# Optimization experiments

Measured on AMD Instinct MI355X. Metric: run time of the kernel, lower is better.

The kernel has to match this reference:

```python
import jax, jax.numpy as jnp
import numpy as np

M, N, DIM = 256, 256, 512
NUM_EPOCHS = 100
ALPHA = 0.3
SIGMA = max(M, N) / 2.0


def _neuron_locations(m, n):
    ii, jj = jnp.meshgrid(jnp.arange(m), jnp.arange(n), indexing='ij')
    return jnp.stack([ii.reshape(-1), jj.reshape(-1)], axis=1)  # [m*n, 2] int32


def setup_inputs() -> dict:
    key = jax.random.key(0)
    k1, k2 = jax.random.split(key)
    input_vector = jax.random.normal(k1, (DIM,), dtype=jnp.float32)
    weights = jax.random.normal(k2, (M * N, DIM), dtype=jnp.float32)
    epoch = 10
    return {"input_vector": input_vector, "weights": weights, "epoch": epoch}


def reference(input_vector, weights, epoch):
    locs = _neuron_locations(M, N)  # [m*n, 2]
    # --- BMU search: broadcast distance + argmin (no tiling needed) ---
    diff = weights - input_vector[None, :]                  # [m*n, dim]
    distance = jnp.sqrt(jnp.sum(diff * diff, axis=1))       # [m*n]
    bmu_index = jnp.argmin(distance)
    bmu_loc = locs[bmu_index]                               # [2]
    # --- training update ---
    epoch_f = jnp.float32(epoch)
    learning_rate = 1.0 - epoch_f / NUM_EPOCHS
    alpha_op = ALPHA * learning_rate
    sigma_op = SIGMA * learning_rate
    loc_diff = locs - bmu_loc[None, :]                      # [m*n, 2]
    bmu_dist_sq = jnp.sum(loc_diff * loc_diff, axis=1).astype(jnp.float32)  # [m*n]
    neighbourhood = jnp.exp(-bmu_dist_sq / (sigma_op * sigma_op))
    lr_mult = (alpha_op * neighbourhood)[:, None]           # [m*n, 1]
    new_weights = weights + lr_mult * (input_vector[None, :] - weights)
    return bmu_loc, new_weights
```

## Files before the change

kernel.cpp:

```cpp
#include <hip/hip_runtime.h>

#define SOM_M 256
#define SOM_N 256
#define SOM_DIM 512
#define SOM_ROWS (SOM_M * SOM_N)
#define SOM_ELEMS (SOM_ROWS * SOM_DIM)
#define NB 2048

typedef float f32x4 __attribute__((ext_vector_type(4)));
typedef float f32x2 __attribute__((ext_vector_type(2)));

__global__ __launch_bounds__(256) void som_bmu_partial(
    const float* __restrict__ w, const float* __restrict__ in,
    unsigned long long* __restrict__ part) {
  __shared__ float s_in[SOM_DIM];
  for (int i = threadIdx.x; i < SOM_DIM; i += 256) s_in[i] = in[i];
  __syncthreads();

  const int wave = threadIdx.x >> 6;
  const int lane = threadIdx.x & 63;
  const int globalWave = blockIdx.x * 4 + wave;
  const int nWaves = NB * 4;

  float bd = 3.4e38f;
  int bi = SOM_ROWS;

  const f32x4* in4 = (const f32x4*)s_in;
  for (int row = globalWave; row < SOM_ROWS; row += nWaves) {
    const f32x4* wr = (const f32x4*)(w + (size_t)row * SOM_DIM);
    float acc = 0.f;
#pragma unroll
    for (int k = 0; k < 2; ++k) {
      f32x4 wv = wr[lane + 64 * k];
      f32x4 iv = in4[lane + 64 * k];
      f32x4 d = wv - iv;
      acc += d.x * d.x + d.y * d.y + d.z * d.z + d.w * d.w;
    }
#pragma unroll
    for (int off = 32; off; off >>= 1) acc += __shfl_xor(acc, off, 64);
    if (acc < bd) { bd = acc; bi = row; }
  }

  unsigned long long pk =
      ((unsigned long long)__float_as_uint(bd) << 32) | (unsigned int)bi;

  __shared__ unsigned long long sp[4];
  if (lane == 0) sp[wave] = pk;
  __syncthreads();
  if (threadIdx.x == 0) {
    unsigned long long m = sp[0];
#pragma unroll
    for (int k = 1; k < 4; ++k) m = (sp[k] < m) ? sp[k] : m;
    part[blockIdx.x] = m;
  }
}

__global__ __launch_bounds__(256) void som_update(
    const float* __restrict__ w, const float* __restrict__ in,
    const int* __restrict__ epoch_p,
    const unsigned long long* __restrict__ part,
    float* __restrict__ out ) {
  __shared__ unsigned long long sp[256];
  unsigned long long m = ~0ull;
  for (int i = threadIdx.x; i < NB; i += 256) {
    unsigned long long v = part[i];
    m = (v < m) ? v : m;
  }
  sp[threadIdx.x] = m;
  __syncthreads();
  for (int s = 128; s; s >>= 1) {
    if ((int)threadIdx.x < s) {
      if (sp[threadIdx.x + s] < sp[threadIdx.x]) sp[threadIdx.x] = sp[threadIdx.x + s];
    }
    __syncthreads();
  }
  const int bidx = (int)(unsigned int)(sp[0] & 0xFFFFFFFFull);
  const int br = bidx >> 8;
  const int bc = bidx & 255;

  if (blockIdx.x == 0 && threadIdx.x == 0) {
    out[0] = (float)br;
    out[1] = (float)bc;
  }

  const float lr = 1.0f - (float)epoch_p[0] / 100.0f;
  const float alpha_op = 0.3f * lr;
  const float sigma_op = 128.0f * lr;
  const float inv_s2 = 1.0f / (sigma_op * sigma_op);

  const f32x2* w2 = (const f32x2*)w;
  const f32x2* in2 = (const f32x2*)in;
  f32x2* o2 = (f32x2*)(out + 2);

  const int total2 = SOM_ELEMS / 2;
  const int stride = NB * 256;
  for (int j = blockIdx.x * 256 + threadIdx.x; j < total2; j += stride) {
    const int row = j >> 8;
    const int rr = (row >> 8) - br;
    const int cc = (row & 255) - bc;
    const float d2 = (float)(rr * rr + cc * cc);
    const float mult = alpha_op * __expf(-d2 * inv_s2);

    f32x2 wv = w2[j];
    f32x2 iv = in2[j & 255];
    f32x2 r = wv + mult * (iv - wv);
    o2[j] = r;
  }
}

extern "C" void kernel_launch(void* const* d_in, const int* in_sizes, int n_in,
                              void* d_out, int out_size, void* d_ws, size_t ws_size,
                              hipStream_t stream) {
  const float* input_vector = (const float*)d_in[0];
  const float* weights = (const float*)d_in[1];
  const int* epoch = (const int*)d_in[2];
  float* out = (float*)d_out;

  unsigned long long* part = (unsigned long long*)d_ws;

  som_bmu_partial<<<NB, 256, 0, stream>>>(weights, input_vector, part);
  som_update<<<NB, 256, 0, stream>>>(weights, input_vector, epoch, part, out);
}
```

Baseline: 69.08 us.

## Fuse BMU search and update into one cooperative kernel holding weights on-chip

Replaces the two-kernel pipeline with a single cooperative-launch kernel. Each wave loads its 32 weight rows once, computes their distances, and keeps the rows in registers (23 rows) and LDS (9 rows). A grid-wide sync and a reduction of the per-wave partial minima then produce the winning neuron, and the update is written from the on-chip copy. This avoids reading the 128MB weight matrix a second time, at the cost of heavy register and LDS pressure, a grid barrier, and reliance on all 512 blocks being co-resident; the old two-kernel path remains as a fallback if the cooperative launch fails.

```diff
diff --git a/kernel.cpp b/kernel.cpp
--- a/kernel.cpp
+++ b/kernel.cpp
@@ -1,30 +1,135 @@
 #include <hip/hip_runtime.h>
-
-#define SOM_M 256
-#define SOM_N 256
+#include <hip/hip_cooperative_groups.h>
+
+namespace cg = cooperative_groups;
+
 #define SOM_DIM 512
-#define SOM_ROWS (SOM_M * SOM_N)
+#define SOM_ROWS 65536
 #define SOM_ELEMS (SOM_ROWS * SOM_DIM)
-#define NB 2048
+
+#define FGRID 512
+#define FWAVES 4
+#define FROWS_PER_WAVE 32
+#define FLDS_ROWS 9
+#define FREG_ROWS 23
+#define FDYN_LDS (FWAVES * FLDS_ROWS * SOM_DIM * 4)
 
 typedef float f32x4 __attribute__((ext_vector_type(4)));
 typedef float f32x2 __attribute__((ext_vector_type(2)));
 
+__global__ __launch_bounds__(256, 2) void som_fused(
+    const float* __restrict__ w, const float* __restrict__ in,
+    const int* __restrict__ epoch_p,
+    unsigned long long* __restrict__ part,
+    float* __restrict__ out) {
+  extern __shared__ float lds[];
+  const int wave = threadIdx.x >> 6;
+  const int lane = threadIdx.x & 63;
+  const int row0 = blockIdx.x * (FWAVES * FROWS_PER_WAVE) + wave * FROWS_PER_WAVE;
+
+  const f32x4* in4 = (const f32x4*)in;
+  const f32x4 iv0 = in4[lane];
+  const f32x4 iv1 = in4[lane + 64];
+
+  float* wlds = lds + wave * (FLDS_ROWS * SOM_DIM);
+
+  float bd = 3.4e38f;
+  int bi = SOM_ROWS;
+  f32x4 d0[FREG_ROWS], d1[FREG_ROWS];
+
+#pragma unroll
+  for (int r = 0; r < FROWS_PER_WAVE; ++r) {
+    const f32x4* wr = (const f32x4*)(w + (size_t)(row0 + r) * SOM_DIM);
+    f32x4 wv0 = wr[lane];
+    f32x4 wv1 = wr[lane + 64];
+    f32x4 e0 = wv0 - iv0;
+    f32x4 e1 = wv1 - iv1;
+    float acc = e0.x * e0.x + e0.y * e0.y + e0.z * e0.z + e0.w * e0.w +
+                e1.x * e1.x + e1.y * e1.y + e1.z * e1.z + e1.w * e1.w;
+#pragma unroll
+    for (int off = 32; off; off >>= 1) acc += __shfl_xor(acc, off, 64);
+    if (acc < bd) { bd = acc; bi = row0 + r; }
+    if (r < FLDS_ROWS) {
+      f32x4* dst = (f32x4*)(wlds + r * SOM_DIM);
+      dst[lane] = wv0;
+      dst[lane + 64] = wv1;
+    } else {
+      d0[r - FLDS_ROWS] = wv0;
+      d1[r - FLDS_ROWS] = wv1;
+    }
+  }
+
+  if (lane == 0) {
+    part[blockIdx.x * FWAVES + wave] =
+        ((unsigned long long)__float_as_uint(bd) << 32) | (unsigned int)bi;
+  }
+
+  cg::this_grid().sync();
+
+  unsigned long long m = part[lane];
+#pragma unroll
+  for (int k = 1; k < 32; ++k) {
+    unsigned long long v = part[lane + 64 * k];
+    m = (v < m) ? v : m;
+  }
+#pragma unroll
+  for (int off = 32; off; off >>= 1) {
+    unsigned long long v = __shfl_xor(m, off, 64);
+    m = (v < m) ? v : m;
+  }
+  const int bidx = (int)(unsigned int)(m & 0xFFFFFFFFull);
+  const int br = bidx >> 8;
+  const int bc = bidx & 255;
+
+  if (blockIdx.x == 0 && threadIdx.x == 0) {
+    out[0] = (float)br;
+    out[1] = (float)bc;
+  }
+
+  const float lr = 1.0f - (float)epoch_p[0] * 0.01f;
+  const float alpha_op = 0.3f * lr;
+  const float sigma_op = 128.0f * lr;
+  const float inv_s2 = 1.0f / (sigma_op * sigma_op);
+
+#pragma unroll
+  for (int r = 0; r < FROWS_PER_WAVE; ++r) {
+    const int row = row0 + r;
+    const int rr = (row >> 8) - br;
+    const int cc = (row & 255) - bc;
+    const float mult = alpha_op * __expf(-(float)(rr * rr + cc * cc) * inv_s2);
+    f32x4 wv0, wv1;
+    if (r < FLDS_ROWS) {
+      const f32x4* src = (const f32x4*)(wlds + r * SOM_DIM);
+      wv0 = src[lane];
+      wv1 = src[lane + 64];
+    } else {
+      wv0 = d0[r - FLDS_ROWS];
+      wv1 = d1[r - FLDS_ROWS];
+    }
+    f32x4 r0 = wv0 + mult * (iv0 - wv0);
+    f32x4 r1 = wv1 + mult * (iv1 - wv1);
+    float* ob = out + 2 + (size_t)row * SOM_DIM;
+    f32x2 a;
+    a.x = r0.x; a.y = r0.y; ((f32x2*)(ob + 4 * lane))[0] = a;
+    a.x = r0.z; a.y = r0.w; ((f32x2*)(ob + 4 * lane + 2))[0] = a;
+    a.x = r1.x; a.y = r1.y; ((f32x2*)(ob + 256 + 4 * lane))[0] = a;
+    a.x = r1.z; a.y = r1.w; ((f32x2*)(ob + 256 + 4 * lane + 2))[0] = a;
+  }
+}
+
+#define NB 2048
 __global__ __launch_bounds__(256) void som_bmu_partial(
     const float* __restrict__ w, const float* __restrict__ in,
     unsigned long long* __restrict__ part) {
   __shared__ float s_in[SOM_DIM];
   for (int i = threadIdx.x; i < SOM_DIM; i += 256) s_in[i] = in[i];
   __syncthreads();
-
   const int wave = threadIdx.x >> 6;
   const int lane = threadIdx.x & 63;
   const int globalWave = blockIdx.x * 4 + wave;
   const int nWaves = NB * 4;
-
   float bd = 3.4e38f;
   int bi = SOM_ROWS;
-
   const f32x4* in4 = (const f32x4*)s_in;
   for (int row = globalWave; row < SOM_ROWS; row += nWaves) {
     const f32x4* wr = (const f32x4*)(w + (size_t)row * SOM_DIM);
@@ -40,18 +145,16 @@
     for (int off = 32; off; off >>= 1) acc += __shfl_xor(acc, off, 64);
     if (acc < bd) { bd = acc; bi = row; }
   }
-
   unsigned long long pk =
       ((unsigned long long)__float_as_uint(bd) << 32) | (unsigned int)bi;
-
   __shared__ unsigned long long sp[4];
   if (lane == 0) sp[wave] = pk;
   __syncthreads();
   if (threadIdx.x == 0) {
-    unsigned long long m = sp[0];
-#pragma unroll
-    for (int k = 1; k < 4; ++k) m = (sp[k] < m) ? sp[k] : m;
-    part[blockIdx.x] = m;
+    unsigned long long mm = sp[0];
+#pragma unroll
+    for (int k = 1; k < 4; ++k) mm = (sp[k] < mm) ? sp[k] : mm;
+    part[blockIdx.x] = mm;
   }
 }
 
@@ -59,7 +162,7 @@
     const float* __restrict__ w, const float* __restrict__ in,
     const int* __restrict__ epoch_p,
     const unsigned long long* __restrict__ part,
-    float* __restrict__ out ) {
+    float* __restrict__ out) {
   __shared__ unsigned long long sp[256];
   unsigned long long m = ~0ull;
   for (int i = threadIdx.x; i < NB; i += 256) {
@@ -77,34 +180,27 @@
   const int bidx = (int)(unsigned int)(sp[0] & 0xFFFFFFFFull);
   const int br = bidx >> 8;
   const int bc = bidx & 255;
-
   if (blockIdx.x == 0 && threadIdx.x == 0) {
     out[0] = (float)br;
     out[1] = (float)bc;
   }
-
-  const float lr = 1.0f - (float)epoch_p[0] / 100.0f;
+  const float lr = 1.0f - (float)epoch_p[0] * 0.01f;
   const float alpha_op = 0.3f * lr;
   const float sigma_op = 128.0f * lr;
   const float inv_s2 = 1.0f / (sigma_op * sigma_op);
-
   const f32x2* w2 = (const f32x2*)w;
   const f32x2* in2 = (const f32x2*)in;
   f32x2* o2 = (f32x2*)(out + 2);
-
   const int total2 = SOM_ELEMS / 2;
   const int stride = NB * 256;
   for (int j = blockIdx.x * 256 + threadIdx.x; j < total2; j += stride) {
     const int row = j >> 8;
     const int rr = (row >> 8) - br;
     const int cc = (row & 255) - bc;
-    const float d2 = (float)(rr * rr + cc * cc);
-    const float mult = alpha_op * __expf(-d2 * inv_s2);
-
+    const float mult = alpha_op * __expf(-(float)(rr * rr + cc * cc) * inv_s2);
     f32x2 wv = w2[j];
     f32x2 iv = in2[j & 255];
-    f32x2 r = wv + mult * (iv - wv);
-    o2[j] = r;
+    o2[j] = wv + mult * (iv - wv);
   }
 }
 
@@ -115,9 +211,18 @@
   const float* weights = (const float*)d_in[1];
   const int* epoch = (const int*)d_in[2];
   float* out = (float*)d_out;
-
   unsigned long long* part = (unsigned long long*)d_ws;
 
-  som_bmu_partial<<<NB, 256, 0, stream>>>(weights, input_vector, part);
-  som_update<<<NB, 256, 0, stream>>>(weights, input_vector, epoch, part, out);
-}
+  (void)hipFuncSetAttribute((const void*)som_fused,
+                            hipFuncAttributeMaxDynamicSharedMemorySize, FDYN_LDS);
+
+  void* kargs[] = {(void*)&weights, (void*)&input_vector, (void*)&epoch,
+                   (void*)&part, (void*)&out};
+  hipError_t e = hipLaunchCooperativeKernel((const void*)som_fused,
+                                            dim3(FGRID), dim3(256), kargs,
+                                            FDYN_LDS, stream);
+  if (e != hipSuccess) {
+    som_bmu_partial<<<NB, 256, 0, stream>>>(weights, input_vector, part);
+    som_update<<<NB, 256, 0, stream>>>(weights, input_vector, epoch, part, out);
+  }
+}
```

New measurement: 173.9 us. 152% more time.

## Fuse BMU search and update into one cooperative kernel with grid sync

Applied to the files above, without the earlier changes.

Replaces the two-kernel pipeline with a single cooperative kernel. Each wave owns 16 contiguous rows, computes their distances, publishes a partial argmin, and waits on a grid-wide sync. After the sync it reduces the partials and updates the same rows in reverse order, so the weight reads in the second pass can hit cache. This removes the second launch and aims to cut the second read of the weights from HBM, at the cost of a grid barrier and a reduction over more partials in every block. The old two-kernel path is kept as a fallback if the cooperative launch fails.

```diff
diff --git a/kernel.cpp b/kernel.cpp
--- a/kernel.cpp
+++ b/kernel.cpp
@@ -1,30 +1,114 @@
 #include <hip/hip_runtime.h>
-
-#define SOM_M 256
-#define SOM_N 256
+#include <hip/hip_cooperative_groups.h>
+
+namespace cg = cooperative_groups;
+
 #define SOM_DIM 512
-#define SOM_ROWS (SOM_M * SOM_N)
+#define SOM_ROWS 65536
 #define SOM_ELEMS (SOM_ROWS * SOM_DIM)
-#define NB 2048
+
+#define FGRID 1024
+#define FWAVES 4
+#define ROWS_PER_WAVE 16
+#define NPART (FGRID * FWAVES)
 
 typedef float f32x4 __attribute__((ext_vector_type(4)));
 typedef float f32x2 __attribute__((ext_vector_type(2)));
-
+typedef unsigned long long u64;
+
+__global__ __launch_bounds__(256, 4) void som_fused(
+    const float* __restrict__ w, const float* __restrict__ in,
+    const int* __restrict__ epoch_p, u64* __restrict__ part,
+    float* __restrict__ out) {
+  const int wave = threadIdx.x >> 6;
+  const int lane = threadIdx.x & 63;
+  const int row0 = blockIdx.x * (FWAVES * ROWS_PER_WAVE) + wave * ROWS_PER_WAVE;
+
+  const f32x2* in2 = (const f32x2*)in;
+  f32x2 iv[4];
+#pragma unroll
+  for (int s = 0; s < 4; ++s) iv[s] = in2[s * 64 + lane];
+
+  float bd = 3.4e38f;
+  int bi = SOM_ROWS;
+
+#pragma unroll 4
+  for (int r = 0; r < ROWS_PER_WAVE; ++r) {
+    const f32x2* wr = (const f32x2*)(w + (size_t)(row0 + r) * SOM_DIM);
+    float acc = 0.f;
+#pragma unroll
+    for (int s = 0; s < 4; ++s) {
+      f32x2 d = wr[s * 64 + lane] - iv[s];
+      acc += d.x * d.x + d.y * d.y;
+    }
+#pragma unroll
+    for (int off = 32; off; off >>= 1) acc += __shfl_xor(acc, off, 64);
+    if (acc < bd) { bd = acc; bi = row0 + r; }
+  }
+
+  if (lane == 0)
+    part[blockIdx.x * FWAVES + wave] =
+        ((u64)__float_as_uint(bd) << 32) | (unsigned int)bi;
+
+  cg::this_grid().sync();
+
+  __shared__ u64 sp[256];
+  u64 m = ~0ull;
+  for (int i = threadIdx.x; i < NPART; i += 256) {
+    u64 v = part[i];
+    m = (v < m) ? v : m;
+  }
+  sp[threadIdx.x] = m;
+  __syncthreads();
+  for (int s = 128; s; s >>= 1) {
+    if ((int)threadIdx.x < s) {
+      if (sp[threadIdx.x + s] < sp[threadIdx.x]) sp[threadIdx.x] = sp[threadIdx.x + s];
+    }
+    __syncthreads();
+  }
+  const int bidx = (int)(unsigned int)(sp[0] & 0xFFFFFFFFull);
+  const int br = bidx >> 8;
+  const int bc = bidx & 255;
+
+  if (blockIdx.x == 0 && threadIdx.x == 0) {
+    out[0] = (float)br;
+    out[1] = (float)bc;
+  }
+
+  const float lr = 1.0f - (float)epoch_p[0] / 100.0f;
+  const float alpha_op = 0.3f * lr;
+  const float sigma_op = 128.0f * lr;
+  const float inv_s2 = 1.0f / (sigma_op * sigma_op);
+
+#pragma unroll 2
+  for (int r = ROWS_PER_WAVE - 1; r >= 0; --r) {
+    const int row = row0 + r;
+    const int rr = (row >> 8) - br;
+    const int cc = (row & 255) - bc;
+    const float mult = alpha_op * __expf(-(float)(rr * rr + cc * cc) * inv_s2);
+    const f32x2* wr = (const f32x2*)(w + (size_t)row * SOM_DIM);
+    f32x2* ob = (f32x2*)(out + 2 + (size_t)row * SOM_DIM);
+#pragma unroll
+    for (int s = 0; s < 4; ++s) {
+      f32x2 wv = wr[s * 64 + lane];
+      ob[s * 64 + lane] = wv + mult * (iv[s] - wv);
+    }
+  }
+}
+
+#define NB 2048
 __global__ __launch_bounds__(256) void som_bmu_partial(
     const float* __restrict__ w, const float* __restrict__ in,
-    unsigned long long* __restrict__ part) {
+    u64* __restrict__ part) {
   __shared__ float s_in[SOM_DIM];
   for (int i = threadIdx.x; i < SOM_DIM; i += 256) s_in[i] = in[i];
   __syncthreads();
-
   const int wave = threadIdx.x >> 6;
   const int lane = threadIdx.x & 63;
   const int globalWave = blockIdx.x * 4 + wave;
   const int nWaves = NB * 4;
-
   float bd = 3.4e38f;
   int bi = SOM_ROWS;
-
   const f32x4* in4 = (const f32x4*)s_in;
   for (int row = globalWave; row < SOM_ROWS; row += nWaves) {
     const f32x4* wr = (const f32x4*)(w + (size_t)row * SOM_DIM);
@@ -40,30 +124,26 @@
     for (int off = 32; off; off >>= 1) acc += __shfl_xor(acc, off, 64);
     if (acc < bd) { bd = acc; bi = row; }
   }
-
-  unsigned long long pk =
-      ((unsigned long long)__float_as_uint(bd) << 32) | (unsigned int)bi;
-
-  __shared__ unsigned long long sp[4];
+  u64 pk = ((u64)__float_as_uint(bd) << 32) | (unsigned int)bi;
+  __shared__ u64 sp[4];
   if (lane == 0) sp[wave] = pk;
   __syncthreads();
   if (threadIdx.x == 0) {
-    unsigned long long m = sp[0];
-#pragma unroll
-    for (int k = 1; k < 4; ++k) m = (sp[k] < m) ? sp[k] : m;
-    part[blockIdx.x] = m;
+    u64 mm = sp[0];
+#pragma unroll
+    for (int k = 1; k < 4; ++k) mm = (sp[k] < mm) ? sp[k] : mm;
+    part[blockIdx.x] = mm;
   }
 }
 
 __global__ __launch_bounds__(256) void som_update(
     const float* __restrict__ w, const float* __restrict__ in,
-    const int* __restrict__ epoch_p,
-    const unsigned long long* __restrict__ part,
-    float* __restrict__ out ) {
-  __shared__ unsigned long long sp[256];
-  unsigned long long m = ~0ull;
+    const int* __restrict__ epoch_p, const u64* __restrict__ part,
+    float* __restrict__ out) {
+  __shared__ u64 sp[256];
+  u64 m = ~0ull;
   for (int i = threadIdx.x; i < NB; i += 256) {
-    unsigned long long v = part[i];
+    u64 v = part[i];
     m = (v < m) ? v : m;
   }
   sp[threadIdx.x] = m;
@@ -77,34 +157,27 @@
   const int bidx = (int)(unsigned int)(sp[0] & 0xFFFFFFFFull);
   const int br = bidx >> 8;
   const int bc = bidx & 255;
-
   if (blockIdx.x == 0 && threadIdx.x == 0) {
     out[0] = (float)br;
     out[1] = (float)bc;
   }
-
   const float lr = 1.0f - (float)epoch_p[0] / 100.0f;
   const float alpha_op = 0.3f * lr;
   const float sigma_op = 128.0f * lr;
   const float inv_s2 = 1.0f / (sigma_op * sigma_op);
-
   const f32x2* w2 = (const f32x2*)w;
   const f32x2* in2 = (const f32x2*)in;
   f32x2* o2 = (f32x2*)(out + 2);
-
   const int total2 = SOM_ELEMS / 2;
   const int stride = NB * 256;
   for (int j = blockIdx.x * 256 + threadIdx.x; j < total2; j += stride) {
     const int row = j >> 8;
     const int rr = (row >> 8) - br;
     const int cc = (row & 255) - bc;
-    const float d2 = (float)(rr * rr + cc * cc);
-    const float mult = alpha_op * __expf(-d2 * inv_s2);
-
+    const float mult = alpha_op * __expf(-(float)(rr * rr + cc * cc) * inv_s2);
     f32x2 wv = w2[j];
     f32x2 iv = in2[j & 255];
-    f32x2 r = wv + mult * (iv - wv);
-    o2[j] = r;
+    o2[j] = wv + mult * (iv - wv);
   }
 }
 
@@ -115,9 +188,15 @@
   const float* weights = (const float*)d_in[1];
   const int* epoch = (const int*)d_in[2];
   float* out = (float*)d_out;
-
-  unsigned long long* part = (unsigned long long*)d_ws;
-
-  som_bmu_partial<<<NB, 256, 0, stream>>>(weights, input_vector, part);
-  som_update<<<NB, 256, 0, stream>>>(weights, input_vector, epoch, part, out);
-}
+  u64* part = (u64*)d_ws;
+
+  void* kargs[] = {(void*)&weights, (void*)&input_vector, (void*)&epoch,
+                   (void*)&part, (void*)&out};
+  hipError_t e = hipLaunchCooperativeKernel((const void*)som_fused,
+                                            dim3(FGRID), dim3(256), kargs,
+                                            0, stream);
+  if (e != hipSuccess) {
+    som_bmu_partial<<<NB, 256, 0, stream>>>(weights, input_vector, part);
+    som_update<<<NB, 256, 0, stream>>>(weights, input_vector, epoch, part, out);
+  }
+}
```

Result: slower. 189.5 us (+174.3%).
